# Kernel tuning notes

Measured on AMD Instinct MI355X. Metric: run time of the kernel, lower is better.

## Reference

```python
import jax, jax.numpy as jnp
import numpy as np

RADII = (3, 5, 7)      # window_levels
S, B, D = 1024, 8, 512  # seq_len, batch, feature_dim
EPS = 1e-12             # F.normalize eps


def setup_inputs() -> dict:
    key = jax.random.key(0)
    k0, k1, k2 = jax.random.split(key, 3)
    x = jax.random.normal(k0, (S, B, D), jnp.float32)          # seq-first like the torch path
    W = jax.random.normal(k1, (3, D, D), jnp.float32) / np.sqrt(D)  # 3 level linear weights
    b = jax.random.normal(k2, (3, D), jnp.float32) * 0.01           # 3 level linear biases
    alphas = jnp.ones((3,), jnp.float32)   # nn.Parameter(torch.ones)
    betas = jnp.zeros((3,), jnp.float32)   # nn.Parameter(torch.zeros)
    return {"x": x, "W": W, "b": b, "alphas": alphas, "betas": betas}


def reference(x, W, b, alphas, betas):
    # x: [S, B, D] (seq-first). torch code transposes to [B, S, D], works, transposes back.
    # Dropout is identity (eval mode). output = x + sum over levels of per-timestep
    # windowed, similarity-weighted sums of linearly transformed neighbors; all
    # windows read the ORIGINAL x, so levels are independent additive terms.
    xb = jnp.transpose(x, (1, 0, 2))  # [B, S, D]
    Bn, Sn, Dn = xb.shape
    dt = xb.dtype
    # L2-normalized features (F.normalize with eps=1e-12)
    xnorm = xb / jnp.maximum(jnp.linalg.norm(xb, axis=-1, keepdims=True), EPS)
    # prefix sums for O(1) window means (edge-truncated windows)
    csum = jnp.concatenate([jnp.zeros((Bn, 1, Dn), dt), jnp.cumsum(xb, axis=1)], axis=1)
    t_idx = jnp.arange(Sn)
    out = xb
    for m, r in enumerate(RADII):
        starts = jnp.clip(t_idx - r, 0, Sn)        # [S]
        ends = jnp.clip(t_idx + r + 1, 0, Sn)      # [S]
        cnt = (ends - starts).astype(dt)           # window sizes (truncated at edges)
        center = (csum[:, ends, :] - csum[:, starts, :]) / cnt[None, :, None]  # [B,S,D]
        cnorm = center / jnp.maximum(jnp.linalg.norm(center, axis=-1, keepdims=True), EPS)
        # sliding-window gather indices, masked at sequence edges
        offs = jnp.arange(-r, r + 1)
        pos = t_idx[:, None] + offs[None, :]       # [S, w]
        valid = ((pos >= 0) & (pos < Sn)).astype(dt)
        idx = jnp.clip(pos, 0, Sn - 1)
        nw = xnorm[:, idx, :]                      # [B, S, w, D]
        sim = jnp.einsum('bswd,bsd->bsw', nw, cnorm)  # cosine similarity to window mean
        wts = jax.nn.sigmoid(alphas[m] * sim + betas[m]) * valid[None, :, :]
        tfm = xb @ W[m].T + b[m]                   # level-m linear transform, computed once
        tw = tfm[:, idx, :]                        # [B, S, w, D]
        out = out + jnp.einsum('bsw,bswd->bsd', wts, tw)
    return jnp.transpose(out, (1, 0, 2))  # back to [S, B, D]
```

## Files before the change

### kernel.cpp

```cpp
#include <hip/hip_runtime.h>

typedef __attribute__((ext_vector_type(8))) short short8;
typedef __attribute__((ext_vector_type(4))) float f32x4;

#define S_LEN 1024
#define B_N 8
#define D_DIM 512
#define SLAB 4194304
#define NX   4194304
#define NW   786432

static __device__ __forceinline__ unsigned short f2bf(float f){
  unsigned int u = __float_as_uint(f);
  u = u + 0x7fffu + ((u>>16)&1u);
  return (unsigned short)(u>>16);
}
static __device__ __forceinline__ float bf2f(unsigned short h){
  return __uint_as_float(((unsigned int)h)<<16);
}

#define GLL16(g,l) __builtin_amdgcn_global_load_lds( \
    (__attribute__((address_space(1))) void*)(g), \
    (__attribute__((address_space(3))) void*)(l), 16, 0, 0)

__global__ __launch_bounds__(256) void k_conv(const float* __restrict__ x,
    const float* __restrict__ W, unsigned short* __restrict__ xbf,
    unsigned short* __restrict__ wbf)
{
  size_t i = ((size_t)blockIdx.x*256 + threadIdx.x)*4;
  const float* src; unsigned short* dst;
  if (i < NX){ src = x + i; dst = xbf + i; }
  else       { src = W + (i - NX); dst = wbf + (i - NX); }
  float4 v = *(const float4*)src;
  ushort4 h;
  h.x = f2bf(v.x); h.y = f2bf(v.y); h.z = f2bf(v.z); h.w = f2bf(v.w);
  *(ushort4*)dst = h;
}

__global__ __launch_bounds__(256) void k_heavy(const unsigned short* __restrict__ A,
    const unsigned short* __restrict__ Bw, const float* __restrict__ bias,
    unsigned short* __restrict__ C, float* __restrict__ Gband)
{
  __shared__ __align__(16) unsigned short smem[16384];
  int blk = blockIdx.x;
  int tid = threadIdx.x, lane = tid & 63, w = tid >> 6;

  if (blk >= 768){
    if (w >= 3) return;
    int g = blk - 768;
    int b = g & 7, i0 = (g >> 3) * 16;
    int j0 = i0 + (w - 1) * 16;
    if (j0 < 0 || j0 >= S_LEN) return;
    int l15 = lane & 15, klo = (lane >> 4) * 8;
    const unsigned short* Ar = A + ((size_t)(i0 + l15) * B_N + b) * D_DIM + klo;
    const unsigned short* Br = A + ((size_t)(j0 + l15) * B_N + b) * D_DIM + klo;
    f32x4 acc = (f32x4){0.f,0.f,0.f,0.f};
    #pragma unroll
    for (int kt = 0; kt < 16; ++kt){
      short8 af = *(const short8*)(Ar + kt*32);
      short8 bf = *(const short8*)(Br + kt*32);
      acc = __builtin_amdgcn_mfma_f32_16x16x32_bf16(af, bf, acc, 0,0,0);
    }
    int rb = (lane >> 4) * 4;
    #pragma unroll
    for (int rg = 0; rg < 4; ++rg){
      int i = i0 + rb + rg;
      int dl = j0 + l15 - i;
      if (dl >= -14 && dl <= 14)
        Gband[((size_t)b * S_LEN + i) * 32 + dl + 14] = acc[rg];
    }
    return;
  }

  unsigned short* As = smem;
  unsigned short* Bs = smem + 4096;
  int bx = blk % 12, by = blk / 12;
  int wm = w >> 1, wn = w & 1;
  int c0 = w*128 + lane, c1 = c0 + 64;
  const unsigned short* gA0 = A + (size_t)(by*128 + (c0>>2))*512 + (c0&3)*8;
  const unsigned short* gA1 = A + (size_t)(by*128 + (c1>>2))*512 + (c1&3)*8;
  const unsigned short* gB0 = Bw + (size_t)(bx*128 + (c0>>2))*512 + (c0&3)*8;
  const unsigned short* gB1 = Bw + (size_t)(bx*128 + (c1>>2))*512 + (c1&3)*8;
  unsigned short* lA0 = As + (w*2+0)*512;
  unsigned short* lA1 = As + (w*2+1)*512;
  unsigned short* lB0 = Bs + (w*2+0)*512;
  unsigned short* lB1 = Bs + (w*2+1)*512;
  f32x4 acc[4][4];
  #pragma unroll
  for (int i=0;i<4;++i)
    #pragma unroll
    for (int j=0;j<4;++j)
      acc[i][j] = (f32x4){0.f,0.f,0.f,0.f};
  int lane15 = lane & 15, klo = (lane>>4)*8;
  for (int kt=0; kt<16; ++kt){
    GLL16(gA0, lA0); GLL16(gA1, lA1); GLL16(gB0, lB0); GLL16(gB1, lB1);
    gA0 += 32; gA1 += 32; gB0 += 32; gB1 += 32;
    __syncthreads();
    short8 af[4], bfr[4];
    #pragma unroll
    for (int i=0;i<4;++i)
      af[i] = *(const short8*)(As + (wm*64 + i*16 + lane15)*32 + klo);
    #pragma unroll
    for (int j=0;j<4;++j)
      bfr[j] = *(const short8*)(Bs + (wn*64 + j*16 + lane15)*32 + klo);
    #pragma unroll
    for (int i=0;i<4;++i)
      #pragma unroll
      for (int j=0;j<4;++j)
        acc[i][j] = __builtin_amdgcn_mfma_f32_16x16x32_bf16(af[i], bfr[j], acc[i][j], 0,0,0);
    __syncthreads();
  }
  int rbase = (lane>>4)*4;
  #pragma unroll
  for (int j=0;j<4;++j){
    int nl = wn*64 + j*16 + lane15;
    float bv = bias[bx*128 + nl];
    #pragma unroll
    for (int i=0;i<4;++i){
      int rl0 = wm*64 + i*16 + rbase;
      #pragma unroll
      for (int rg=0;rg<4;++rg)
        smem[(rl0+rg)*128 + nl] = f2bf(acc[i][j][rg] + bv);
    }
  }
  __syncthreads();
  int m_r = bx >> 2, colb = (bx&3)*128;
  #pragma unroll
  for (int p=0;p<8;++p){
    int R = p*16 + (tid>>4);
    int ch = (tid&15)*8;
    uint4 v = *(const uint4*)(smem + R*128 + ch);
    *(uint4*)(C + (size_t)m_r*SLAB + (size_t)(by*128 + R)*512 + colb + ch) = v;
  }
}

__global__ __launch_bounds__(256) void k_gath(const float* __restrict__ x,
    const unsigned short* __restrict__ tfm, const float* __restrict__ Gband,
    const float* __restrict__ alphas, const float* __restrict__ betas,
    float* __restrict__ out)
{
  int blk = blockIdx.x;
  int b = blk & 7, tg = blk >> 3;
  int tid = threadIdx.x, h = tid >> 7, j = tid & 127;
  int t = tg * 2 + h;
  __shared__ float pshare[2][33];
  __shared__ float invc[2][3];
  __shared__ float wsh[2][33];
  int m = 0, pos = 0, valid = 0;
  float pp = 0.f, invnp = 0.f;
  if (j < 33){
    int r, wsl;
    if (j < 7){ m = 0; r = 3; wsl = j; }
    else if (j < 18){ m = 1; r = 5; wsl = j - 7; }
    else { m = 2; r = 7; wsl = j - 18; }
    pos = t + wsl - r;
    valid = (pos >= 0 && pos < S_LEN);
    if (valid){
      const float* grow = Gband + ((size_t)b * S_LEN + pos) * 32;
      int ulo = max(t - r, 0), uhi = min(t + r, S_LEN - 1);
      for (int u = ulo; u <= uhi; ++u) pp += grow[u - pos + 14];
      invnp = rsqrtf(fmaxf(grow[14], 1e-24f));
    }
    pshare[h][j] = valid ? pp : 0.f;
  }
  __syncthreads();
  if (j < 3){
    int s0 = j == 0 ? 0 : (j == 1 ? 7 : 18);
    int c  = j == 0 ? 7 : (j == 1 ? 11 : 15);
    float s = 0.f;
    for (int k = 0; k < c; ++k) s += pshare[h][s0 + k];
    invc[h][j] = rsqrtf(fmaxf(s, 1e-24f));
  }
  __syncthreads();
  if (j < 33){
    float wt = 0.f;
    if (valid){
      float sim = pp * invnp * invc[h][m];
      float z = alphas[m] * sim + betas[m];
      wt = 1.0f / (1.0f + expf(-z));
    }
    wsh[h][j] = wt;
  }
  __syncthreads();
  int d0 = j * 4;
  size_t xoff = ((size_t)t * B_N + b) * D_DIM + d0;
  float4 a = *(const float4*)(x + xoff);
  float ax = a.x, ay = a.y, az = a.z, aw = a.w;
  #pragma unroll
  for (int p = 0; p < 33; ++p){
    int pm, pr, wsl;
    if (p < 7){ pm = 0; pr = 3; wsl = p; }
    else if (p < 18){ pm = 1; pr = 5; wsl = p - 7; }
    else { pm = 2; pr = 7; wsl = p - 18; }
    int ppos = t + wsl - pr;
    if (ppos < 0 || ppos >= S_LEN) continue;
    float wt = wsh[h][p];
    const unsigned short* tp = tfm + (size_t)pm * SLAB + ((size_t)ppos * B_N + b) * D_DIM + d0;
    uint2 uv = *(const uint2*)tp;
    ax += wt * bf2f((unsigned short)(uv.x & 0xffffu));
    ay += wt * bf2f((unsigned short)(uv.x >> 16));
    az += wt * bf2f((unsigned short)(uv.y & 0xffffu));
    aw += wt * bf2f((unsigned short)(uv.y >> 16));
  }
  *(float4*)(out + xoff) = make_float4(ax, ay, az, aw);
}

extern "C" void kernel_launch(void* const* d_in, const int* in_sizes, int n_in,
                              void* d_out, int out_size, void* d_ws, size_t ws_size,
                              hipStream_t stream) {
  const float* x      = (const float*)d_in[0];
  const float* W      = (const float*)d_in[1];
  const float* bias   = (const float*)d_in[2];
  const float* alphas = (const float*)d_in[3];
  const float* betas  = (const float*)d_in[4];
  float* out = (float*)d_out;
  char* ws = (char*)d_ws;
  unsigned short* xbf  = (unsigned short*)ws;
  unsigned short* wbf  = (unsigned short*)(ws + 8388608);
  unsigned short* tfm  = (unsigned short*)(ws + 8388608 + 1572864);
  float*          Gband= (float*)(ws + 8388608 + 1572864 + 25165824);

  k_conv <<<4864, 256, 0, stream>>>(x, W, xbf, wbf);
  k_heavy<<<1280, 256, 0, stream>>>(xbf, wbf, bias, tfm, Gband);
  k_gath <<<4096, 256, 0, stream>>>(x, tfm, Gband, alphas, betas, out);
}
```

Baseline: 67.81 us.

## Reorder to weighted-sum-then-GEMM, folding bias via weight sums

The computation is reassociated so each level's windowed, similarity-weighted sum is taken over raw x first. A single K=1536 GEMM against the concatenated bf16 weights then applies the linear transforms, with bias added as the sum of weights times b. This removes the separate x-to-bf16 conversion pass and the 24 MB bf16 tfm intermediate write and read. The Gram band now converts fp32 x to bf16 on the fly, and the trade is a larger bf16 y intermediate (three slabs) plus a final GEMM with a fused epilogue, using 64x128 tiles in a 512-block grid.

```diff
diff --git a/kernel.cpp b/kernel.cpp
--- a/kernel.cpp
+++ b/kernel.cpp
@@ -6,8 +6,8 @@
 #define S_LEN 1024
 #define B_N 8
 #define D_DIM 512
-#define SLAB 4194304
-#define NX   4194304
+#define SLAB_Y 4194304
+#define SLAB_W 262144
 #define NW   786432
 
 static __device__ __forceinline__ unsigned short f2bf(float f){
@@ -15,129 +15,61 @@
   u = u + 0x7fffu + ((u>>16)&1u);
   return (unsigned short)(u>>16);
 }
-static __device__ __forceinline__ float bf2f(unsigned short h){
-  return __uint_as_float(((unsigned int)h)<<16);
-}
 
 #define GLL16(g,l) __builtin_amdgcn_global_load_lds( \
     (__attribute__((address_space(1))) void*)(g), \
     (__attribute__((address_space(3))) void*)(l), 16, 0, 0)
 
-__global__ __launch_bounds__(256) void k_conv(const float* __restrict__ x,
-    const float* __restrict__ W, unsigned short* __restrict__ xbf,
+__global__ __launch_bounds__(256) void k_gramw(const float* __restrict__ x,
+    const float* __restrict__ W, float* __restrict__ Gband,
     unsigned short* __restrict__ wbf)
 {
-  size_t i = ((size_t)blockIdx.x*256 + threadIdx.x)*4;
-  const float* src; unsigned short* dst;
-  if (i < NX){ src = x + i; dst = xbf + i; }
-  else       { src = W + (i - NX); dst = wbf + (i - NX); }
-  float4 v = *(const float4*)src;
-  ushort4 h;
-  h.x = f2bf(v.x); h.y = f2bf(v.y); h.z = f2bf(v.z); h.w = f2bf(v.w);
-  *(ushort4*)dst = h;
-}
-
-__global__ __launch_bounds__(256) void k_heavy(const unsigned short* __restrict__ A,
-    const unsigned short* __restrict__ Bw, const float* __restrict__ bias,
-    unsigned short* __restrict__ C, float* __restrict__ Gband)
-{
-  __shared__ __align__(16) unsigned short smem[16384];
   int blk = blockIdx.x;
-  int tid = threadIdx.x, lane = tid & 63, w = tid >> 6;
-
-  if (blk >= 768){
-    if (w >= 3) return;
-    int g = blk - 768;
-    int b = g & 7, i0 = (g >> 3) * 16;
-    int j0 = i0 + (w - 1) * 16;
-    if (j0 < 0 || j0 >= S_LEN) return;
-    int l15 = lane & 15, klo = (lane >> 4) * 8;
-    const unsigned short* Ar = A + ((size_t)(i0 + l15) * B_N + b) * D_DIM + klo;
-    const unsigned short* Br = A + ((size_t)(j0 + l15) * B_N + b) * D_DIM + klo;
-    f32x4 acc = (f32x4){0.f,0.f,0.f,0.f};
-    #pragma unroll
-    for (int kt = 0; kt < 16; ++kt){
-      short8 af = *(const short8*)(Ar + kt*32);
-      short8 bf = *(const short8*)(Br + kt*32);
-      acc = __builtin_amdgcn_mfma_f32_16x16x32_bf16(af, bf, acc, 0,0,0);
-    }
-    int rb = (lane >> 4) * 4;
-    #pragma unroll
-    for (int rg = 0; rg < 4; ++rg){
-      int i = i0 + rb + rg;
-      int dl = j0 + l15 - i;
-      if (dl >= -14 && dl <= 14)
-        Gband[((size_t)b * S_LEN + i) * 32 + dl + 14] = acc[rg];
-    }
+  int tid = threadIdx.x;
+  if (blk >= 512){
+    int i = ((blk - 512)*256 + tid)*4;
+    float4 v = *(const float4*)(W + i);
+    ushort4 hh;
+    hh.x = f2bf(v.x); hh.y = f2bf(v.y); hh.z = f2bf(v.z); hh.w = f2bf(v.w);
+    *(ushort4*)(wbf + i) = hh;
     return;
   }
-
-  unsigned short* As = smem;
-  unsigned short* Bs = smem + 4096;
-  int bx = blk % 12, by = blk / 12;
-  int wm = w >> 1, wn = w & 1;
-  int c0 = w*128 + lane, c1 = c0 + 64;
-  const unsigned short* gA0 = A + (size_t)(by*128 + (c0>>2))*512 + (c0&3)*8;
-  const unsigned short* gA1 = A + (size_t)(by*128 + (c1>>2))*512 + (c1&3)*8;
-  const unsigned short* gB0 = Bw + (size_t)(bx*128 + (c0>>2))*512 + (c0&3)*8;
-  const unsigned short* gB1 = Bw + (size_t)(bx*128 + (c1>>2))*512 + (c1&3)*8;
-  unsigned short* lA0 = As + (w*2+0)*512;
-  unsigned short* lA1 = As + (w*2+1)*512;
-  unsigned short* lB0 = Bs + (w*2+0)*512;
-  unsigned short* lB1 = Bs + (w*2+1)*512;
-  f32x4 acc[4][4];
-  #pragma unroll
-  for (int i=0;i<4;++i)
-    #pragma unroll
-    for (int j=0;j<4;++j)
-      acc[i][j] = (f32x4){0.f,0.f,0.f,0.f};
-  int lane15 = lane & 15, klo = (lane>>4)*8;
-  for (int kt=0; kt<16; ++kt){
-    GLL16(gA0, lA0); GLL16(gA1, lA1); GLL16(gB0, lB0); GLL16(gB1, lB1);
-    gA0 += 32; gA1 += 32; gB0 += 32; gB1 += 32;
-    __syncthreads();
-    short8 af[4], bfr[4];
-    #pragma unroll
-    for (int i=0;i<4;++i)
-      af[i] = *(const short8*)(As + (wm*64 + i*16 + lane15)*32 + klo);
-    #pragma unroll
-    for (int j=0;j<4;++j)
-      bfr[j] = *(const short8*)(Bs + (wn*64 + j*16 + lane15)*32 + klo);
-    #pragma unroll
-    for (int i=0;i<4;++i)
-      #pragma unroll
-      for (int j=0;j<4;++j)
-        acc[i][j] = __builtin_amdgcn_mfma_f32_16x16x32_bf16(af[i], bfr[j], acc[i][j], 0,0,0);
-    __syncthreads();
-  }
-  int rbase = (lane>>4)*4;
-  #pragma unroll
-  for (int j=0;j<4;++j){
-    int nl = wn*64 + j*16 + lane15;
-    float bv = bias[bx*128 + nl];
-    #pragma unroll
-    for (int i=0;i<4;++i){
-      int rl0 = wm*64 + i*16 + rbase;
-      #pragma unroll
-      for (int rg=0;rg<4;++rg)
-        smem[(rl0+rg)*128 + nl] = f2bf(acc[i][j][rg] + bv);
-    }
-  }
-  __syncthreads();
-  int m_r = bx >> 2, colb = (bx&3)*128;
-  #pragma unroll
-  for (int p=0;p<8;++p){
-    int R = p*16 + (tid>>4);
-    int ch = (tid&15)*8;
-    uint4 v = *(const uint4*)(smem + R*128 + ch);
-    *(uint4*)(C + (size_t)m_r*SLAB + (size_t)(by*128 + R)*512 + colb + ch) = v;
-  }
-}
-
-__global__ __launch_bounds__(256) void k_gath(const float* __restrict__ x,
-    const unsigned short* __restrict__ tfm, const float* __restrict__ Gband,
-    const float* __restrict__ alphas, const float* __restrict__ betas,
-    float* __restrict__ out)
+  int lane = tid & 63, w = tid >> 6;
+  if (w >= 3) return;
+  int b = blk & 7, i0 = (blk >> 3) * 16;
+  int j0 = i0 + (w - 1) * 16;
+  if (j0 < 0 || j0 >= S_LEN) return;
+  int l15 = lane & 15, klo = (lane >> 4) * 8;
+  const float* Ar = x + ((size_t)(i0 + l15) * B_N + b) * D_DIM + klo;
+  const float* Br = x + ((size_t)(j0 + l15) * B_N + b) * D_DIM + klo;
+  f32x4 acc = (f32x4){0.f,0.f,0.f,0.f};
+  #pragma unroll
+  for (int kt = 0; kt < 16; ++kt){
+    float4 a0 = *(const float4*)(Ar + kt*32);
+    float4 a1 = *(const float4*)(Ar + kt*32 + 4);
+    float4 b0 = *(const float4*)(Br + kt*32);
+    float4 b1 = *(const float4*)(Br + kt*32 + 4);
+    short8 af, bf;
+    af[0]=f2bf(a0.x); af[1]=f2bf(a0.y); af[2]=f2bf(a0.z); af[3]=f2bf(a0.w);
+    af[4]=f2bf(a1.x); af[5]=f2bf(a1.y); af[6]=f2bf(a1.z); af[7]=f2bf(a1.w);
+    bf[0]=f2bf(b0.x); bf[1]=f2bf(b0.y); bf[2]=f2bf(b0.z); bf[3]=f2bf(b0.w);
+    bf[4]=f2bf(b1.x); bf[5]=f2bf(b1.y); bf[6]=f2bf(b1.z); bf[7]=f2bf(b1.w);
+    acc = __builtin_amdgcn_mfma_f32_16x16x32_bf16(af, bf, acc, 0,0,0);
+  }
+  int rb = (lane >> 4) * 4;
+  #pragma unroll
+  for (int rg = 0; rg < 4; ++rg){
+    int i = i0 + rb + rg;
+    int dl = j0 + l15 - i;
+    if (dl >= -14 && dl <= 14)
+      Gband[((size_t)b * S_LEN + i) * 32 + dl + 14] = acc[rg];
+  }
+}
+
+__global__ __launch_bounds__(256) void k_wsum(const float* __restrict__ x,
+    const float* __restrict__ Gband, const float* __restrict__ alphas,
+    const float* __restrict__ betas, unsigned short* __restrict__ y,
+    float* __restrict__ sw)
 {
   int blk = blockIdx.x;
   int b = blk & 7, tg = blk >> 3;
@@ -182,10 +114,18 @@
     wsh[h][j] = wt;
   }
   __syncthreads();
+  size_t row = (size_t)t * B_N + b;
+  if (j < 3){
+    int s0 = j == 0 ? 0 : (j == 1 ? 7 : 18);
+    int c  = j == 0 ? 7 : (j == 1 ? 11 : 15);
+    float s = 0.f;
+    for (int k = 0; k < c; ++k) s += wsh[h][s0 + k];
+    sw[(size_t)j * 8192 + row] = s;
+  }
   int d0 = j * 4;
-  size_t xoff = ((size_t)t * B_N + b) * D_DIM + d0;
-  float4 a = *(const float4*)(x + xoff);
-  float ax = a.x, ay = a.y, az = a.z, aw = a.w;
+  f32x4 y0 = (f32x4){0.f,0.f,0.f,0.f};
+  f32x4 y1 = (f32x4){0.f,0.f,0.f,0.f};
+  f32x4 y2 = (f32x4){0.f,0.f,0.f,0.f};
   #pragma unroll
   for (int p = 0; p < 33; ++p){
     int pm, pr, wsl;
@@ -195,14 +135,106 @@
     int ppos = t + wsl - pr;
     if (ppos < 0 || ppos >= S_LEN) continue;
     float wt = wsh[h][p];
-    const unsigned short* tp = tfm + (size_t)pm * SLAB + ((size_t)ppos * B_N + b) * D_DIM + d0;
-    uint2 uv = *(const uint2*)tp;
-    ax += wt * bf2f((unsigned short)(uv.x & 0xffffu));
-    ay += wt * bf2f((unsigned short)(uv.x >> 16));
-    az += wt * bf2f((unsigned short)(uv.y & 0xffffu));
-    aw += wt * bf2f((unsigned short)(uv.y >> 16));
-  }
-  *(float4*)(out + xoff) = make_float4(ax, ay, az, aw);
+    const float* xp = x + ((size_t)ppos * B_N + b) * D_DIM + d0;
+    float4 xv = *(const float4*)xp;
+    if (pm == 0){ y0[0]+=wt*xv.x; y0[1]+=wt*xv.y; y0[2]+=wt*xv.z; y0[3]+=wt*xv.w; }
+    else if (pm == 1){ y1[0]+=wt*xv.x; y1[1]+=wt*xv.y; y1[2]+=wt*xv.z; y1[3]+=wt*xv.w; }
+    else { y2[0]+=wt*xv.x; y2[1]+=wt*xv.y; y2[2]+=wt*xv.z; y2[3]+=wt*xv.w; }
+  }
+  ushort4 h0, h1, h2;
+  h0.x=f2bf(y0[0]); h0.y=f2bf(y0[1]); h0.z=f2bf(y0[2]); h0.w=f2bf(y0[3]);
+  h1.x=f2bf(y1[0]); h1.y=f2bf(y1[1]); h1.z=f2bf(y1[2]); h1.w=f2bf(y1[3]);
+  h2.x=f2bf(y2[0]); h2.y=f2bf(y2[1]); h2.z=f2bf(y2[2]); h2.w=f2bf(y2[3]);
+  *(ushort4*)(y + 0*(size_t)SLAB_Y + row*D_DIM + d0) = h0;
+  *(ushort4*)(y + 1*(size_t)SLAB_Y + row*D_DIM + d0) = h1;
+  *(ushort4*)(y + 2*(size_t)SLAB_Y + row*D_DIM + d0) = h2;
+}
+
+__global__ __launch_bounds__(256) void k_gemm(const unsigned short* __restrict__ y,
+    const unsigned short* __restrict__ wbf, const float* __restrict__ x,
+    const float* __restrict__ bias, const float* __restrict__ sw,
+    float* __restrict__ out)
+{
+  __shared__ __align__(16) unsigned char smem[32768];
+  unsigned short* As = (unsigned short*)smem;
+  unsigned short* Bs = As + 2048;
+  float* Ct = (float*)smem;
+  int blk = blockIdx.x;
+  int bx = blk & 3, by = blk >> 2;
+  int tid = threadIdx.x, lane = tid & 63, w = tid >> 6;
+  int wm = w >> 1, wn = w & 1;
+  int ca = w*64 + lane;
+  int cb1 = w*64 + lane;
+  int cb2 = 256 + w*64 + lane;
+  const unsigned short* g0 = y   + ((size_t)(by*64  + (ca>>2)))*512 + (ca&3)*8;
+  const unsigned short* g1 = wbf + ((size_t)(bx*128 + (cb1>>2)))*512 + (cb1&3)*8;
+  const unsigned short* g2 = wbf + ((size_t)(bx*128 + (cb2>>2)))*512 + (cb2&3)*8;
+  unsigned short* l0 = As + w*512;
+  unsigned short* l1 = Bs + w*512;
+  unsigned short* l2 = Bs + 2048 + w*512;
+  f32x4 acc[2][4];
+  #pragma unroll
+  for (int i=0;i<2;++i)
+    #pragma unroll
+    for (int jj=0;jj<4;++jj)
+      acc[i][jj] = (f32x4){0.f,0.f,0.f,0.f};
+  int l15 = lane & 15, klo = (lane>>4)*8;
+  for (int mslab = 0; mslab < 3; ++mslab){
+    for (int kt = 0; kt < 16; ++kt){
+      GLL16(g0, l0); GLL16(g1, l1); GLL16(g2, l2);
+      g0 += 32; g1 += 32; g2 += 32;
+      __syncthreads();
+      short8 af[2], bfr[4];
+      #pragma unroll
+      for (int i=0;i<2;++i)
+        af[i] = *(const short8*)(As + (wm*32 + i*16 + l15)*32 + klo);
+      #pragma unroll
+      for (int jj=0;jj<4;++jj)
+        bfr[jj] = *(const short8*)(Bs + (wn*64 + jj*16 + l15)*32 + klo);
+      #pragma unroll
+      for (int i=0;i<2;++i)
+        #pragma unroll
+        for (int jj=0;jj<4;++jj)
+          acc[i][jj] = __builtin_amdgcn_mfma_f32_16x16x32_bf16(af[i], bfr[jj], acc[i][jj], 0,0,0);
+      __syncthreads();
+    }
+    if (mslab < 2){
+      g0 += (size_t)SLAB_Y - 512;
+      g1 += (size_t)SLAB_W - 512;
+      g2 += (size_t)SLAB_W - 512;
+    }
+  }
+  int rbase = (lane>>4)*4;
+  #pragma unroll
+  for (int jj=0;jj<4;++jj){
+    int col = wn*64 + jj*16 + l15;
+    #pragma unroll
+    for (int i=0;i<2;++i){
+      int r0 = wm*32 + i*16 + rbase;
+      #pragma unroll
+      for (int rg=0;rg<4;++rg)
+        Ct[(r0+rg)*128 + col] = acc[i][jj][rg];
+    }
+  }
+  __syncthreads();
+  #pragma unroll
+  for (int q=0;q<8;++q){
+    int R = q*8 + (tid>>5);
+    int ch = (tid&31)*4;
+    int grow = by*64 + R, gcol = bx*128 + ch;
+    float4 cv = *(const float4*)(Ct + R*128 + ch);
+    float4 xv = *(const float4*)(x + (size_t)grow*512 + gcol);
+    float s0 = sw[grow], s1 = sw[8192 + grow], s2 = sw[16384 + grow];
+    float4 b0 = *(const float4*)(bias + gcol);
+    float4 b1 = *(const float4*)(bias + 512 + gcol);
+    float4 b2 = *(const float4*)(bias + 1024 + gcol);
+    float4 ov;
+    ov.x = xv.x + cv.x + s0*b0.x + s1*b1.x + s2*b2.x;
+    ov.y = xv.y + cv.y + s0*b0.y + s1*b1.y + s2*b2.y;
+    ov.z = xv.z + cv.z + s0*b0.z + s1*b1.z + s2*b2.z;
+    ov.w = xv.w + cv.w + s0*b0.w + s1*b1.w + s2*b2.w;
+    *(float4*)(out + (size_t)grow*512 + gcol) = ov;
+  }
 }
 
 extern "C" void kernel_launch(void* const* d_in, const int* in_sizes, int n_in,
@@ -215,12 +247,12 @@
   const float* betas  = (const float*)d_in[4];
   float* out = (float*)d_out;
   char* ws = (char*)d_ws;
-  unsigned short* xbf  = (unsigned short*)ws;
-  unsigned short* wbf  = (unsigned short*)(ws + 8388608);
-  unsigned short* tfm  = (unsigned short*)(ws + 8388608 + 1572864);
-  float*          Gband= (float*)(ws + 8388608 + 1572864 + 25165824);
-
-  k_conv <<<4864, 256, 0, stream>>>(x, W, xbf, wbf);
-  k_heavy<<<1280, 256, 0, stream>>>(xbf, wbf, bias, tfm, Gband);
-  k_gath <<<4096, 256, 0, stream>>>(x, tfm, Gband, alphas, betas, out);
-}
+  unsigned short* wbf  = (unsigned short*)ws;
+  float*          Gband= (float*)(ws + 1572864);
+  unsigned short* y    = (unsigned short*)(ws + 1572864 + 1048576);
+  float*          sw   = (float*)(ws + 1572864 + 1048576 + 25165824);
+
+  k_gramw<<<1280, 256, 0, stream>>>(x, W, Gband, wbf);
+  k_wsum <<<4096, 256, 0, stream>>>(x, Gband, alphas, betas, y, sw);
+  k_gemm <<< 512, 256, 0, stream>>>(y, wbf, x, bias, sw, out);
+}
```

After: 74.15 us. 9.3% more time.

## Double-buffer GEMM LDS tiles to overlap global loads with MFMA

Applied to the files above, without the earlier changes.

The tiled GEMM in k_heavy now keeps two LDS buffers and issues the async global-to-LDS loads for the next k-tile before computing on the current one. One hand-placed barrier and one vmcnt wait per iteration replace the two __syncthreads. The aim is to hide global load latency behind the MFMA work. It uses the full 32KB of shared memory already declared, and it depends on explicit waitcnt and sched_barrier ordering being correct.

```diff
diff --git a/kernel.cpp b/kernel.cpp
--- a/kernel.cpp
+++ b/kernel.cpp
@@ -8,7 +8,6 @@
 #define D_DIM 512
 #define SLAB 4194304
 #define NX   4194304
-#define NW   786432
 
 static __device__ __forceinline__ unsigned short f2bf(float f){
   unsigned int u = __float_as_uint(f);
@@ -22,6 +21,11 @@
 #define GLL16(g,l) __builtin_amdgcn_global_load_lds( \
     (__attribute__((address_space(1))) void*)(g), \
     (__attribute__((address_space(3))) void*)(l), 16, 0, 0)
+
+#define SBAR() do { __builtin_amdgcn_sched_barrier(0); \
+  asm volatile("s_barrier" ::: "memory"); \
+  __builtin_amdgcn_sched_barrier(0); } while(0)
+#define VMCNT0() asm volatile("s_waitcnt vmcnt(0)" ::: "memory")
 
 __global__ __launch_bounds__(256) void k_conv(const float* __restrict__ x,
     const float* __restrict__ W, unsigned short* __restrict__ xbf,
@@ -72,8 +76,6 @@
     return;
   }
 
-  unsigned short* As = smem;
-  unsigned short* Bs = smem + 4096;
   int bx = blk % 12, by = blk / 12;
   int wm = w >> 1, wn = w & 1;
   int c0 = w*128 + lane, c1 = c0 + 64;
@@ -81,39 +83,52 @@
   const unsigned short* gA1 = A + (size_t)(by*128 + (c1>>2))*512 + (c1&3)*8;
   const unsigned short* gB0 = Bw + (size_t)(bx*128 + (c0>>2))*512 + (c0&3)*8;
   const unsigned short* gB1 = Bw + (size_t)(bx*128 + (c1>>2))*512 + (c1&3)*8;
-  unsigned short* lA0 = As + (w*2+0)*512;
-  unsigned short* lA1 = As + (w*2+1)*512;
-  unsigned short* lB0 = Bs + (w*2+0)*512;
-  unsigned short* lB1 = Bs + (w*2+1)*512;
   f32x4 acc[4][4];
   #pragma unroll
   for (int i=0;i<4;++i)
     #pragma unroll
     for (int j=0;j<4;++j)
       acc[i][j] = (f32x4){0.f,0.f,0.f,0.f};
-  int lane15 = lane & 15, klo = (lane>>4)*8;
-  for (int kt=0; kt<16; ++kt){
-    GLL16(gA0, lA0); GLL16(gA1, lA1); GLL16(gB0, lB0); GLL16(gB1, lB1);
+  int l15 = lane & 15, klo = (lane>>4)*8;
+  {
+    unsigned short* s0 = smem + w*1024;
+    GLL16(gA0, s0); GLL16(gA1, s0 + 512);
+    GLL16(gB0, s0 + 4096); GLL16(gB1, s0 + 4096 + 512);
     gA0 += 32; gA1 += 32; gB0 += 32; gB1 += 32;
-    __syncthreads();
+  }
+  VMCNT0(); SBAR();
+  #pragma unroll
+  for (int kt = 0; kt < 16; ++kt){
+    unsigned short* sc = smem + (kt & 1)*8192;
+    if (kt < 15){
+      unsigned short* sn = smem + ((kt + 1) & 1)*8192 + w*1024;
+      GLL16(gA0, sn); GLL16(gA1, sn + 512);
+      GLL16(gB0, sn + 4096); GLL16(gB1, sn + 4096 + 512);
+      gA0 += 32; gA1 += 32; gB0 += 32; gB1 += 32;
+    }
     short8 af[4], bfr[4];
     #pragma unroll
     for (int i=0;i<4;++i)
-      af[i] = *(const short8*)(As + (wm*64 + i*16 + lane15)*32 + klo);
+      af[i] = *(const short8*)(sc + (wm*64 + i*16 + l15)*32 + klo);
     #pragma unroll
     for (int j=0;j<4;++j)
-      bfr[j] = *(const short8*)(Bs + (wn*64 + j*16 + lane15)*32 + klo);
+      bfr[j] = *(const short8*)(sc + 4096 + (wn*64 + j*16 + l15)*32 + klo);
     #pragma unroll
     for (int i=0;i<4;++i)
       #pragma unroll
       for (int j=0;j<4;++j)
         acc[i][j] = __builtin_amdgcn_mfma_f32_16x16x32_bf16(af[i], bfr[j], acc[i][j], 0,0,0);
-    __syncthreads();
-  }
+    if (kt < 15){
+      __builtin_amdgcn_sched_barrier(0);
+      VMCNT0();
+      SBAR();
+    }
+  }
+  __syncthreads();
   int rbase = (lane>>4)*4;
   #pragma unroll
   for (int j=0;j<4;++j){
-    int nl = wn*64 + j*16 + lane15;
+    int nl = wn*64 + j*16 + l15;
     float bv = bias[bx*128 + nl];
     #pragma unroll
     for (int i=0;i<4;++i){
```

Result: faster. 65.58 us (-3.3%).
